# Kernel optimization log

Hardware: AMD Instinct MI355X
Metric: run time of the kernel (lower is better)

## Reference

```python
import jax, jax.numpy as jnp
import numpy as np

B, S, D = 2, 1024, 1024
L, E, F = 2, 8, 2048


def setup_inputs() -> dict:
    key = jax.random.key(0)
    kx, kp, k1, k2 = jax.random.split(key, 4)
    x = jax.random.normal(kx, (B, S, D), dtype=jnp.float32)
    # prototypes scaled so dot products are O(1), keeping softmax well-behaved
    protos = jax.random.normal(kp, (L, E, D), dtype=jnp.float32) / np.sqrt(D)
    W1 = jax.random.normal(k1, (L, E, D, F), dtype=jnp.float32) * 0.02
    W2 = jax.random.normal(k2, (L, E, F, D), dtype=jnp.float32) * 0.02
    return {"x": x, "protos": protos, "W1": W1, "W2": W2, "k": 2}


def _route(x, protos_l, k):
    # expert_mapping: abs(dot(prototype, input)) per expert, keep top-k, rest -> -inf, softmax
    scores = jnp.abs(jnp.einsum("bsd,ed->bse", x, protos_l))  # [B,S,E]
    topv, _ = jax.lax.top_k(scores, k)
    thresh = topv[..., -1:]  # k-th largest per token
    masked = jnp.where(scores >= thresh, scores, -jnp.inf)
    return jax.nn.softmax(masked, axis=-1)  # [B,S,E]


def reference(x, protos, W1, W2, k):
    n_layers = protos.shape[0]
    for l in range(n_layers):  # fixed small layer loop
        w = _route(x, protos[l], k)  # [B,S,E]
        h = jax.nn.relu(jnp.einsum("bsd,edf->bsef", x, W1[l]))  # [B,S,E,F]
        y = jnp.einsum("bsef,efd,bse->bsd", h, W2[l], w)  # weighted expert mix
        x = x + y
    return x
```

## Files before the change

### kernel.cpp

```cpp
#include <hip/hip_runtime.h>
#include <hip/hip_bf16.h>
#include <cstdint>

#define T_TOKENS 2048
#define DDIM 1024
#define FDIM 2048
#define NEXP 8
#define NLAYER 2
#define BMPAD 64
#define RMAX 4608
#define RALLOC 4736

#define ATILE_EL 2048
#define BTILE_EL 4096

typedef unsigned short u16;
typedef short bf16x8 __attribute__((ext_vector_type(8)));
typedef u16 u16x8 __attribute__((ext_vector_type(8)));
typedef u16 u16x4v __attribute__((ext_vector_type(4)));
typedef float f32x4 __attribute__((ext_vector_type(4)));

__device__ __forceinline__ u16 bf16_rn(float f) {
  unsigned u = __builtin_bit_cast(unsigned, f);
  u += 0x7fffu + ((u >> 16) & 1u);
  return (u16)(u >> 16);
}
__device__ __forceinline__ float bf16_f(u16 h) {
  unsigned u = ((unsigned)h) << 16;
  return __builtin_bit_cast(float, u);
}

__device__ __forceinline__ void gl16(const void* g, void* l) {
  __builtin_amdgcn_global_load_lds((const __attribute__((address_space(1))) void*)g,
                                   (__attribute__((address_space(3))) void*)l, 16, 0, 0);
}

__device__ __forceinline__ void xcd_swizzle(int& bx, int& by, int& bz) {
  const unsigned gx = gridDim.x, gy = gridDim.y;
  const unsigned lin = blockIdx.x + gx * (blockIdx.y + gy * blockIdx.z);
  const unsigned nwg = gx * gy * gridDim.z;
  const unsigned nl = (lin & 7u) * (nwg >> 3) + (lin >> 3);
  bx = nl % gx;
  const unsigned t = nl / gx;
  by = t % gy;
  bz = t / gy;
}

__global__ __launch_bounds__(256) void route_kernel(
    const float* __restrict__ x, const float* __restrict__ protos,
    int* __restrict__ eid, float* __restrict__ wgt) {
  const int t = blockIdx.x;
  const int tid = threadIdx.x;
  const float4* xr4 = (const float4*)(x + (size_t)t * DDIM);
  const float4* pr4 = (const float4*)protos;
  __shared__ float red[NEXP][256];
  const float4 xv = xr4[tid];
  float acc[NEXP];
#pragma unroll
  for (int e = 0; e < NEXP; ++e) {
    const float4 p = pr4[e * 256 + tid];
    acc[e] = xv.x * p.x + xv.y * p.y + xv.z * p.z + xv.w * p.w;
  }
#pragma unroll
  for (int e = 0; e < NEXP; ++e) red[e][tid] = acc[e];
  __syncthreads();
  for (int s = 128; s > 0; s >>= 1) {
    if (tid < s) {
#pragma unroll
      for (int e = 0; e < NEXP; ++e) red[e][tid] += red[e][tid + s];
    }
    __syncthreads();
  }
  if (tid == 0) {
    float m1 = -1.f, m2 = -1.f;
    int i1 = 0, i2 = 0;
#pragma unroll
    for (int e = 0; e < NEXP; ++e) {
      float s = fabsf(red[e][0]);
      if (s > m1) { m2 = m1; i2 = i1; m1 = s; i1 = e; }
      else if (s > m2) { m2 = s; i2 = e; }
    }
    float e2 = __expf(m2 - m1);
    float z = 1.f + e2;
    eid[t * 2] = i1;
    eid[t * 2 + 1] = i2;
    wgt[t * 2] = 1.f / z;
    wgt[t * 2 + 1] = e2 / z;
  }
}

__global__ __launch_bounds__(256) void route2_kernel(
    const float* __restrict__ x, const float* __restrict__ protos2,
    const u16* __restrict__ h_hi, const u16* __restrict__ h_lo,
    const float* __restrict__ P, const int* __restrict__ eidA,
    const int* __restrict__ pos, const float* __restrict__ wgtA,
    int* __restrict__ eidB, float* __restrict__ wgtB) {
  const int t = blockIdx.x;
  const int tid = threadIdx.x;
  __shared__ float red[NEXP][256];
  const float4 xv = ((const float4*)(x + (size_t)t * DDIM))[tid];
  float acc[NEXP];
#pragma unroll
  for (int e = 0; e < NEXP; ++e) {
    const float4 p = ((const float4*)protos2)[e * 256 + tid];
    acc[e] = xv.x * p.x + xv.y * p.y + xv.z * p.z + xv.w * p.w;
  }
  const int p0 = pos[t * 2], p1 = pos[t * 2 + 1];
  const int e0 = eidA[t * 2], e1 = eidA[t * 2 + 1];
  const float w0 = wgtA[t * 2], w1 = wgtA[t * 2 + 1];
  const int f0 = tid * 8;
  const int nkbF = FDIM >> 5;
  float h0[8], h1[8];
  {
    const size_t el0 = ((size_t)(p0 >> 6) * nkbF + (f0 >> 5)) * ATILE_EL +
                       (size_t)((((f0 >> 3) & 3) * 64 + (p0 & 63)) * 8);
    const size_t el1 = ((size_t)(p1 >> 6) * nkbF + (f0 >> 5)) * ATILE_EL +
                       (size_t)((((f0 >> 3) & 3) * 64 + (p1 & 63)) * 8);
    u16x8 a = *(const u16x8*)&h_hi[el0], b = *(const u16x8*)&h_lo[el0];
    u16x8 c = *(const u16x8*)&h_hi[el1], d = *(const u16x8*)&h_lo[el1];
#pragma unroll
    for (int j = 0; j < 8; ++j) {
      h0[j] = bf16_f(a[j]) + bf16_f(b[j]);
      h1[j] = bf16_f(c[j]) + bf16_f(d[j]);
    }
  }
#pragma unroll
  for (int e2 = 0; e2 < NEXP; ++e2) {
    const float* P0 = P + ((size_t)(e0 * NEXP + e2)) * FDIM + f0;
    const float* P1 = P + ((size_t)(e1 * NEXP + e2)) * FDIM + f0;
    float c = 0.f;
#pragma unroll
    for (int j = 0; j < 8; ++j) c += w0 * h0[j] * P0[j] + w1 * h1[j] * P1[j];
    acc[e2] += c;
  }
#pragma unroll
  for (int e = 0; e < NEXP; ++e) red[e][tid] = acc[e];
  __syncthreads();
  for (int s = 128; s > 0; s >>= 1) {
    if (tid < s) {
#pragma unroll
      for (int e = 0; e < NEXP; ++e) red[e][tid] += red[e][tid + s];
    }
    __syncthreads();
  }
  if (tid == 0) {
    float m1 = -1.f, m2 = -1.f;
    int i1 = 0, i2 = 0;
#pragma unroll
    for (int e = 0; e < NEXP; ++e) {
      float s = fabsf(red[e][0]);
      if (s > m1) { m2 = m1; i2 = i1; m1 = s; i1 = e; }
      else if (s > m2) { m2 = s; i2 = e; }
    }
    float e2 = __expf(m2 - m1);
    float z = 1.f + e2;
    eidB[t * 2] = i1;
    eidB[t * 2 + 1] = i2;
    wgtB[t * 2] = 1.f / z;
    wgtB[t * 2 + 1] = e2 / z;
  }
}

__global__ __launch_bounds__(256) void compact_kernel(
    const int* __restrict__ eid, int* __restrict__ cnt, int* __restrict__ offp,
    int* __restrict__ row2token, int* __restrict__ pos) {
  __shared__ int lcnt[NEXP][256];
  __shared__ int s_off[NEXP], s_tot[NEXP];
  const int tid = threadIdx.x;
  const int base = tid * 16;

  int my[16];
#pragma unroll
  for (int i = 0; i < 4; ++i)
    *(int4*)&my[i * 4] = *(const int4*)(eid + base + i * 4);

#pragma unroll
  for (int e = 0; e < NEXP; ++e) {
    int c = 0;
#pragma unroll
    for (int i = 0; i < 16; ++i) c += (my[i] == e) ? 1 : 0;
    lcnt[e][tid] = c;
  }

  for (int r = tid; r < RMAX; r += 256) row2token[r] = -1;
  __syncthreads();

  if (tid < NEXP) {
    int run = 0;
    for (int i = 0; i < 256; ++i) {
      int v = lcnt[tid][i];
      lcnt[tid][i] = run;
      run += v;
    }
    s_tot[tid] = run;
  }
  __syncthreads();
  if (tid == 0) {
    int o = 0;
    for (int e = 0; e < NEXP; ++e) {
      s_off[e] = o;
      o += (s_tot[e] + BMPAD - 1) & ~(BMPAD - 1);
    }
  }
  __syncthreads();

  int myoff[NEXP];
#pragma unroll
  for (int e = 0; e < NEXP; ++e) myoff[e] = s_off[e] + lcnt[e][tid];
#pragma unroll
  for (int i = 0; i < 16; ++i) {
    int r = 0;
#pragma unroll
    for (int e = 0; e < NEXP; ++e) r = (my[i] == e) ? myoff[e] : r;
    row2token[r] = (base + i) >> 1;
    pos[base + i] = r;
#pragma unroll
    for (int e = 0; e < NEXP; ++e) myoff[e] += (my[i] == e) ? 1 : 0;
  }

  if (tid < NEXP) {
    cnt[tid] = s_tot[tid];
    offp[tid] = s_off[tid];
  }
}

template <bool LO>
__global__ __launch_bounds__(256) void gather_kernel(
    const float* __restrict__ x, const int* __restrict__ row2token,
    u16* __restrict__ Ahi, u16* __restrict__ Alo) {
  const int r = blockIdx.x;
  const int t = row2token[r];
  const int c = threadIdx.x * 4;
  float4 v = make_float4(0.f, 0.f, 0.f, 0.f);
  if (t >= 0) v = *(const float4*)(x + (size_t)t * DDIM + c);
  float vv[4] = {v.x, v.y, v.z, v.w};
  u16x4v hi, lo;
#pragma unroll
  for (int i = 0; i < 4; ++i) {
    u16 h = bf16_rn(vv[i]);
    hi[i] = h;
    if (LO) lo[i] = bf16_rn(vv[i] - bf16_f(h));
  }
  const size_t el = ((size_t)(r >> 6) * (DDIM >> 5) + (c >> 5)) * ATILE_EL +
                    (size_t)(((c >> 3) & 3) * 64 + (r & 63)) * 8 + (c & 7);
  *(u16x4v*)(Ahi + el) = hi;
  if (LO) *(u16x4v*)(Alo + el) = lo;
}

template <bool LO>
__global__ __launch_bounds__(256) void wconv_kernel(
    const float* __restrict__ W, u16* __restrict__ Hi, u16* __restrict__ Lo,
    int K, int N) {
  const int e = blockIdx.z, nb = blockIdx.x, kb = blockIdx.y;
  const float* Wp = W + ((size_t)e * K + (size_t)kb * 32) * N + nb * 128;
  __shared__ float tile[32][129];
  const int t = threadIdx.x;
#pragma unroll
  for (int i = 0; i < 4; ++i) {
    const int f4 = i * 256 + t;
    const int kr = f4 >> 5;
    const int c4 = (f4 & 31) * 4;
    float4 v = *(const float4*)(Wp + (size_t)kr * N + c4);
    *(float4*)&tile[kr][c4] = v;
  }
  __syncthreads();
  const size_t tb = (((size_t)e * (N >> 7) + nb) * (K >> 5) + kb) * BTILE_EL;
#pragma unroll
  for (int j = 0; j < 2; ++j) {
    const int cid = j * 256 + t;
    const int n = cid & 127, ksel = cid >> 7;
    u16x8 hv, lv;
#pragma unroll
    for (int i = 0; i < 8; ++i) {
      float f = tile[ksel * 8 + i][n];
      u16 h = bf16_rn(f);
      hv[i] = h;
      if (LO) lv[i] = bf16_rn(f - bf16_f(h));
    }
    *(u16x8*)(Hi + tb + (size_t)cid * 8) = hv;
    if (LO) *(u16x8*)(Lo + tb + (size_t)cid * 8) = lv;
  }
}

__global__ __launch_bounds__(256) void wconv_p_kernel(
    const float* __restrict__ W, u16* __restrict__ Hi,
    const float* __restrict__ proto2, float* __restrict__ Ppart, int K, int N) {
  const int e = blockIdx.z, nb = blockIdx.x, kb = blockIdx.y;
  const float* Wp = W + ((size_t)e * K + (size_t)kb * 32) * N + nb * 128;
  __shared__ float tile[32][129];
  __shared__ float pr[NEXP][128];
  const int t = threadIdx.x;
#pragma unroll
  for (int i = 0; i < 4; ++i) {
    const int f4 = i * 256 + t;
    const int kr = f4 >> 5;
    const int c4 = (f4 & 31) * 4;
    float4 v = *(const float4*)(Wp + (size_t)kr * N + c4);
    *(float4*)&tile[kr][c4] = v;
  }
  {
    const int idx = t * 4;
    const int e2 = idx >> 7, n = idx & 127;
    *(float4*)&pr[e2][n] = *(const float4*)(proto2 + (size_t)e2 * DDIM + nb * 128 + n);
  }
  __syncthreads();
  const size_t tb = (((size_t)e * (N >> 7) + nb) * (K >> 5) + kb) * BTILE_EL;
#pragma unroll
  for (int j = 0; j < 2; ++j) {
    const int cid = j * 256 + t;
    const int n = cid & 127, ksel = cid >> 7;
    u16x8 hv;
#pragma unroll
    for (int i = 0; i < 8; ++i) hv[i] = bf16_rn(tile[ksel * 8 + i][n]);
    *(u16x8*)(Hi + tb + (size_t)cid * 8) = hv;
  }
  const int e2 = t >> 5, f = t & 31;
  float s = 0.f;
#pragma unroll 16
  for (int n = 0; n < 128; ++n) s += tile[f][n] * pr[e2][n];
  Ppart[(((size_t)nb * NEXP + e) * NEXP + e2) * FDIM + kb * 32 + f] = s;
}

__global__ __launch_bounds__(256) void reduce_p_kernel(
    const float* __restrict__ Ppart, float* __restrict__ P) {
  const int i = blockIdx.x * 256 + threadIdx.x;
  float s = 0.f;
#pragma unroll
  for (int nb = 0; nb < 8; ++nb) s += Ppart[(size_t)nb * (NEXP * NEXP * FDIM) + i];
  P[i] = s;
}

__global__ __launch_bounds__(256, 3) void gemm_split(
    const u16* __restrict__ Ahi, const u16* __restrict__ Alo,
    const u16* __restrict__ Bhi, const u16* __restrict__ Blo,
    u16* __restrict__ OutHi, u16* __restrict__ OutLo,
    const int* __restrict__ cnt, const int* __restrict__ offp, int K, int N) {
  int bx, by, bz;
  xcd_swizzle(bx, by, bz);
  const int e = bz;
  const int cp = (cnt[e] + 63) & ~63;
  if (by * 64 >= cp) return;
  const int row0 = offp[e] + by * 64;
  const int n0 = bx * 128;
  const int nkb = K >> 5;

  constexpr int BUF_EL = 12288;
  __shared__ u16 lds[2 * BUF_EL];

  const int tid = threadIdx.x;
  const int lane = tid & 63;
  const int wid = tid >> 6;
  const int wr = wid >> 1, wc = wid & 1;
  const int lr = lane & 15, kg = lane >> 4;
  const int lo16 = lane << 4;

  f32x4 acc[2][4];
#pragma unroll
  for (int i = 0; i < 2; ++i)
#pragma unroll
    for (int j = 0; j < 4; ++j)
#pragma unroll
      for (int r = 0; r < 4; ++r) acc[i][j][r] = 0.f;

  const size_t abase = (size_t)(row0 >> 6) * nkb;
  const size_t bbase = ((size_t)e * (N >> 7) + (n0 >> 7)) * nkb;

  auto STAGE = [&](int kb, int b) {
    char* d = (char*)(lds + b * BUF_EL);
    if (wid == 0) {
      const char* gh = (const char*)(Ahi + (abase + kb) * ATILE_EL);
      const char* gl = (const char*)(Alo + (abase + kb) * ATILE_EL);
#pragma unroll
      for (int i = 0; i < 4; ++i) gl16(gh + i * 1024 + lo16, d + i * 1024);
#pragma unroll
      for (int i = 0; i < 4; ++i) gl16(gl + i * 1024 + lo16, d + 4096 + i * 1024);
    } else if (wid == 1) {
      const char* g = (const char*)(Bhi + (bbase + kb) * BTILE_EL);
#pragma unroll
      for (int i = 0; i < 8; ++i) gl16(g + i * 1024 + lo16, d + 8192 + i * 1024);
    } else if (wid == 2) {
      const char* g = (const char*)(Blo + (bbase + kb) * BTILE_EL);
#pragma unroll
      for (int i = 0; i < 8; ++i) gl16(g + i * 1024 + lo16, d + 16384 + i * 1024);
    }
  };

  STAGE(0, 0);
  __syncthreads();

  int cur = 0;
  for (int kb = 0; kb < nkb; ++kb) {
    if (kb + 1 < nkb) STAGE(kb + 1, cur ^ 1);

    const u16* buf = lds + cur * BUF_EL;
    const u16* AsH = buf;
    const u16* AsL = buf + 2048;
    const u16* BsH = buf + 4096;
    const u16* BsL = buf + 8192;
    const int arow = (kg * 64 + wr * 32 + lr) * 8;
    const int bcol = (kg * 128 + wc * 64 + lr) * 8;

    bf16x8 ah0 = *(const bf16x8*)&AsH[arow];
    bf16x8 ah1 = *(const bf16x8*)&AsH[arow + 128];
    bf16x8 bh[4];
#pragma unroll
    for (int j = 0; j < 4; ++j) bh[j] = *(const bf16x8*)&BsH[bcol + j * 128];
#pragma unroll
    for (int j = 0; j < 4; ++j) {
      acc[0][j] = __builtin_amdgcn_mfma_f32_16x16x32_bf16(ah0, bh[j], acc[0][j], 0, 0, 0);
      acc[1][j] = __builtin_amdgcn_mfma_f32_16x16x32_bf16(ah1, bh[j], acc[1][j], 0, 0, 0);
    }
    bf16x8 al0 = *(const bf16x8*)&AsL[arow];
    bf16x8 al1 = *(const bf16x8*)&AsL[arow + 128];
#pragma unroll
    for (int j = 0; j < 4; ++j) {
      bf16x8 bl = *(const bf16x8*)&BsL[bcol + j * 128];
      acc[0][j] = __builtin_amdgcn_mfma_f32_16x16x32_bf16(ah0, bl, acc[0][j], 0, 0, 0);
      acc[1][j] = __builtin_amdgcn_mfma_f32_16x16x32_bf16(ah1, bl, acc[1][j], 0, 0, 0);
      acc[0][j] = __builtin_amdgcn_mfma_f32_16x16x32_bf16(al0, bh[j], acc[0][j], 0, 0, 0);
      acc[1][j] = __builtin_amdgcn_mfma_f32_16x16x32_bf16(al1, bh[j], acc[1][j], 0, 0, 0);
    }
    __syncthreads();
    cur ^= 1;
  }

  const int nkbO = N >> 5;
#pragma unroll
  for (int i = 0; i < 2; ++i) {
#pragma unroll
    for (int j = 0; j < 4; ++j) {
      const int Cj = n0 + wc * 64 + j * 16 + lr;
      f32x4 v = acc[i][j];
#pragma unroll
      for (int r = 0; r < 4; ++r) {
        const int R = row0 + wr * 32 + i * 16 + kg * 4 + r;
        float f = fmaxf(v[r], 0.f);
        const size_t el = ((size_t)(R >> 6) * nkbO + (Cj >> 5)) * ATILE_EL +
                          (size_t)(((Cj >> 3) & 3) * 64 + (R & 63)) * 8 + (Cj & 7);
        u16 h = bf16_rn(f);
        OutHi[el] = h;
        OutLo[el] = bf16_rn(f - bf16_f(h));
      }
    }
  }
}

template <bool RELU, int OUTMODE, int SKF>
__global__ __launch_bounds__(256, 4) void gemm_plain(
    const u16* __restrict__ Ahi, const u16* __restrict__ Bhi,
    u16* __restrict__ OutHi, float* __restrict__ OutF,
    const int* __restrict__ cnt, const int* __restrict__ offp, int K, int N) {
  int bx, by, bz;
  xcd_swizzle(bx, by, bz);
  const int e = bz / SKF, sk = bz % SKF;
  const int cp = (cnt[e] + 63) & ~63;
  if (by * 128 >= cp) return;
  const int row0 = offp[e] + by * 128;
  const int rend = offp[e] + cp;
  const int n0 = bx * 128;
  const int nkb = K >> 5;
  const int kbN = nkb / SKF;
  const int kb0 = sk * kbN;

  constexpr int BUF_EL = 8192;
  __shared__ u16 lds[2 * BUF_EL];

  const int tid = threadIdx.x;
  const int lane = tid & 63;
  const int wid = tid >> 6;
  const int wr = wid >> 1, wc = wid & 1;
  const int lr = lane & 15, kg = lane >> 4;
  const int lo16 = lane << 4;

  f32x4 acc[4][4];
#pragma unroll
  for (int i = 0; i < 4; ++i)
#pragma unroll
    for (int j = 0; j < 4; ++j)
#pragma unroll
      for (int r = 0; r < 4; ++r) acc[i][j][r] = 0.f;

  const int at0 = row0 >> 6;
  const size_t bbase = ((size_t)e * (N >> 7) + (n0 >> 7)) * nkb;

  auto STAGE = [&](int kb, int b) {
    char* d = (char*)(lds + b * BUF_EL);
    if (wid < 2) {
      const char* g = (const char*)(Ahi + ((size_t)(at0 + wid) * nkb + kb) * ATILE_EL);
#pragma unroll
      for (int i = 0; i < 4; ++i) gl16(g + i * 1024 + lo16, d + wid * 4096 + i * 1024);
    } else {
      const char* g = (const char*)(Bhi + (bbase + kb) * BTILE_EL) + (wid - 2) * 4096;
#pragma unroll
      for (int i = 0; i < 4; ++i) gl16(g + i * 1024 + lo16, d + 8192 + (wid - 2) * 4096 + i * 1024);
    }
  };

  STAGE(kb0, 0);
  __syncthreads();

  int cur = 0;
  for (int kb = kb0; kb < kb0 + kbN; ++kb) {
    if (kb + 1 < kb0 + kbN) STAGE(kb + 1, cur ^ 1);

    const u16* buf = lds + cur * BUF_EL;
    const u16* AsH = buf + wr * 2048;
    const u16* BsH = buf + 4096;
    const int arow = (kg * 64 + lr) * 8;
    const int bcol = (kg * 128 + wc * 64 + lr) * 8;

    bf16x8 ah[4], bh[4];
#pragma unroll
    for (int i = 0; i < 4; ++i) ah[i] = *(const bf16x8*)&AsH[arow + i * 128];
#pragma unroll
    for (int j = 0; j < 4; ++j) bh[j] = *(const bf16x8*)&BsH[bcol + j * 128];
#pragma unroll
    for (int i = 0; i < 4; ++i)
#pragma unroll
      for (int j = 0; j < 4; ++j)
        acc[i][j] = __builtin_amdgcn_mfma_f32_16x16x32_bf16(ah[i], bh[j], acc[i][j], 0, 0, 0);
    __syncthreads();
    cur ^= 1;
  }

  const int nkbO = N >> 5;
#pragma unroll
  for (int i = 0; i < 4; ++i) {
#pragma unroll
    for (int j = 0; j < 4; ++j) {
      const int Cj = n0 + wc * 64 + j * 16 + lr;
      f32x4 v = acc[i][j];
#pragma unroll
      for (int r = 0; r < 4; ++r) {
        const int R = row0 + wr * 64 + i * 16 + kg * 4 + r;
        if (R >= rend) continue;
        float f = v[r];
        if (RELU) f = fmaxf(f, 0.f);
        if constexpr (OUTMODE == 0) {
          OutF[((size_t)sk * RALLOC + R) * N + Cj] = f;
        } else {
          const size_t el = ((size_t)(R >> 6) * nkbO + (Cj >> 5)) * ATILE_EL +
                            (size_t)(((Cj >> 3) & 3) * 64 + (R & 63)) * 8 + (Cj & 7);
          OutHi[el] = bf16_rn(f);
        }
      }
    }
  }
}

__global__ __launch_bounds__(256) void apply_kernel(
    const float* __restrict__ part, const int* __restrict__ pos,
    const float* __restrict__ wgt, float* __restrict__ x) {
  const int t = blockIdx.x;
  const int c = threadIdx.x * 4;
  const int p0 = pos[t * 2], p1 = pos[t * 2 + 1];
  const float w0 = wgt[t * 2], w1 = wgt[t * 2 + 1];
  const float* P1p = part + (size_t)RALLOC * DDIM;
  float4 xa = *(float4*)(x + (size_t)t * DDIM + c);
  float4 y0 = *(const float4*)(part + (size_t)p0 * DDIM + c);
  float4 y1 = *(const float4*)(part + (size_t)p1 * DDIM + c);
  const float4 b0 = *(const float4*)(P1p + (size_t)p0 * DDIM + c);
  const float4 b1 = *(const float4*)(P1p + (size_t)p1 * DDIM + c);
  y0.x += b0.x; y0.y += b0.y; y0.z += b0.z; y0.w += b0.w;
  y1.x += b1.x; y1.y += b1.y; y1.z += b1.z; y1.w += b1.w;
  xa.x += w0 * y0.x + w1 * y1.x;
  xa.y += w0 * y0.y + w1 * y1.y;
  xa.z += w0 * y0.z + w1 * y1.z;
  xa.w += w0 * y0.w + w1 * y1.w;
  *(float4*)(x + (size_t)t * DDIM + c) = xa;
}

extern "C" void kernel_launch(void* const* d_in, const int* in_sizes, int n_in,
                              void* d_out, int out_size, void* d_ws, size_t ws_size,
                              hipStream_t stream) {
  const float* x = (const float*)d_in[0];
  const float* protos = (const float*)d_in[1];
  const float* W1 = (const float*)d_in[2];
  const float* W2 = (const float*)d_in[3];
  float* xcur = (float*)d_out;

  u16* W_hi = (u16*)d_ws;
  u16* W_lo = W_hi + (size_t)NEXP * DDIM * FDIM;
  u16* Ag_hi = W_lo + (size_t)NEXP * DDIM * FDIM;
  u16* Ag_lo = Ag_hi + (size_t)RALLOC * DDIM;
  u16* h_hi = Ag_lo + (size_t)RALLOC * DDIM;
  u16* h_lo = h_hi + (size_t)RALLOC * FDIM;
  float* part = (float*)(h_lo + (size_t)RALLOC * FDIM);
  float* Ppart = part + (size_t)2 * RALLOC * DDIM;
  float* P = Ppart + (size_t)8 * NEXP * NEXP * FDIM;
  float* wgtA = P + (size_t)NEXP * NEXP * FDIM;
  float* wgtB = wgtA + T_TOKENS * 2;
  int* eidA = (int*)(wgtB + T_TOKENS * 2);
  int* eidB = eidA + T_TOKENS * 2;
  int* posA = eidB + T_TOKENS * 2;
  int* posB = posA + T_TOKENS * 2;
  int* cnt = posB + T_TOKENS * 2;
  int* offp = cnt + NEXP;
  int* row2token = offp + NEXP;

  hipMemcpyAsync(xcur, x, (size_t)T_TOKENS * DDIM * sizeof(float),
                 hipMemcpyDeviceToDevice, stream);

  const float* protos2 = protos + (size_t)NEXP * DDIM;

  route_kernel<<<T_TOKENS, 256, 0, stream>>>(xcur, protos, eidA, wgtA);
  compact_kernel<<<1, 256, 0, stream>>>(eidA, cnt, offp, row2token, posA);
  gather_kernel<true><<<RMAX, 256, 0, stream>>>(xcur, row2token, Ag_hi, Ag_lo);
  wconv_kernel<true><<<dim3(FDIM / 128, DDIM / 32, NEXP), 256, 0, stream>>>(
      W1, W_hi, W_lo, DDIM, FDIM);
  gemm_split<<<dim3(FDIM / 128, RMAX / 64, NEXP), 256, 0, stream>>>(
      Ag_hi, Ag_lo, W_hi, W_lo, h_hi, h_lo, cnt, offp, DDIM, FDIM);
  wconv_p_kernel<<<dim3(DDIM / 128, FDIM / 32, NEXP), 256, 0, stream>>>(
      W2, W_hi, protos2, Ppart, FDIM, DDIM);
  reduce_p_kernel<<<NEXP * NEXP * FDIM / 256, 256, 0, stream>>>(Ppart, P);
  gemm_plain<false, 0, 2><<<dim3(DDIM / 128, RMAX / 128, NEXP * 2), 256, 0, stream>>>(
      h_hi, W_hi, nullptr, part, cnt, offp, FDIM, DDIM);
  route2_kernel<<<T_TOKENS, 256, 0, stream>>>(
      xcur, protos2, h_hi, h_lo, P, eidA, posA, wgtA, eidB, wgtB);
  apply_kernel<<<T_TOKENS, 256, 0, stream>>>(part, posA, wgtA, xcur);

  compact_kernel<<<1, 256, 0, stream>>>(eidB, cnt, offp, row2token, posB);
  gather_kernel<false><<<RMAX, 256, 0, stream>>>(xcur, row2token, Ag_hi, nullptr);
  wconv_kernel<false><<<dim3(FDIM / 128, DDIM / 32, NEXP), 256, 0, stream>>>(
      W1 + (size_t)NEXP * DDIM * FDIM, W_hi, nullptr, DDIM, FDIM);
  gemm_plain<true, 2, 1><<<dim3(FDIM / 128, RMAX / 128, NEXP), 256, 0, stream>>>(
      Ag_hi, W_hi, h_hi, nullptr, cnt, offp, DDIM, FDIM);
  wconv_kernel<false><<<dim3(DDIM / 128, FDIM / 32, NEXP), 256, 0, stream>>>(
      W2 + (size_t)NEXP * FDIM * DDIM, W_hi, nullptr, FDIM, DDIM);
  gemm_plain<false, 0, 2><<<dim3(DDIM / 128, RMAX / 128, NEXP * 2), 256, 0, stream>>>(
      h_hi, W_hi, nullptr, part, cnt, offp, FDIM, DDIM);
  apply_kernel<<<T_TOKENS, 256, 0, stream>>>(part, posB, wgtB, xcur);
}
```

Before: 366.7 us.

## Balance async LDS staging across all waves and use partial vmcnt waits

The tile-loading work in both GEMM kernels is spread evenly across all four waves, each issuing the same number of global-to-LDS loads, where before one wave carried the A load and three carried uneven B loads. __syncthreads is replaced with explicit s_waitcnt vmcnt(N) plus raw s_barrier and sched barriers. This lets the next stage's prefetch stay in flight while the current buffer is consumed, instead of draining all outstanding loads at each barrier. It depends on the vmcnt counts being exactly right; a wrong count would race on LDS.

```diff
diff --git a/kernel.cpp b/kernel.cpp
--- a/kernel.cpp
+++ b/kernel.cpp
@@ -19,6 +19,10 @@
 typedef u16 u16x8 __attribute__((ext_vector_type(8)));
 typedef u16 u16x4v __attribute__((ext_vector_type(4)));
 typedef float f32x4 __attribute__((ext_vector_type(4)));
+
+#define VMCNT(n) asm volatile("s_waitcnt vmcnt(" #n ")" ::: "memory")
+#define SB() __builtin_amdgcn_sched_barrier(0)
+#define BAR() __builtin_amdgcn_s_barrier()
 
 __device__ __forceinline__ u16 bf16_rn(float f) {
   unsigned u = __builtin_bit_cast(unsigned, f);
@@ -367,30 +371,48 @@
 
   auto STAGE = [&](int kb, int b) {
     char* d = (char*)(lds + b * BUF_EL);
+    const char* gah = (const char*)(Ahi + (abase + kb) * ATILE_EL);
+    const char* gal = (const char*)(Alo + (abase + kb) * ATILE_EL);
+    const char* gbh = (const char*)(Bhi + (bbase + kb) * BTILE_EL);
+    const char* gbl = (const char*)(Blo + (bbase + kb) * BTILE_EL);
     if (wid == 0) {
-      const char* gh = (const char*)(Ahi + (abase + kb) * ATILE_EL);
-      const char* gl = (const char*)(Alo + (abase + kb) * ATILE_EL);
-#pragma unroll
-      for (int i = 0; i < 4; ++i) gl16(gh + i * 1024 + lo16, d + i * 1024);
-#pragma unroll
-      for (int i = 0; i < 4; ++i) gl16(gl + i * 1024 + lo16, d + 4096 + i * 1024);
+      gl16(gah + 0 * 1024 + lo16, d + 0 * 1024);
+      gl16(gah + 1 * 1024 + lo16, d + 1 * 1024);
+      gl16(gah + 2 * 1024 + lo16, d + 2 * 1024);
+      gl16(gah + 3 * 1024 + lo16, d + 3 * 1024);
+      gl16(gal + 0 * 1024 + lo16, d + 4096 + 0 * 1024);
+      gl16(gal + 1 * 1024 + lo16, d + 4096 + 1 * 1024);
     } else if (wid == 1) {
-      const char* g = (const char*)(Bhi + (bbase + kb) * BTILE_EL);
-#pragma unroll
-      for (int i = 0; i < 8; ++i) gl16(g + i * 1024 + lo16, d + 8192 + i * 1024);
+      gl16(gal + 2 * 1024 + lo16, d + 4096 + 2 * 1024);
+      gl16(gal + 3 * 1024 + lo16, d + 4096 + 3 * 1024);
+      gl16(gbh + 0 * 1024 + lo16, d + 8192 + 0 * 1024);
+      gl16(gbh + 1 * 1024 + lo16, d + 8192 + 1 * 1024);
+      gl16(gbh + 2 * 1024 + lo16, d + 8192 + 2 * 1024);
+      gl16(gbh + 3 * 1024 + lo16, d + 8192 + 3 * 1024);
     } else if (wid == 2) {
-      const char* g = (const char*)(Blo + (bbase + kb) * BTILE_EL);
-#pragma unroll
-      for (int i = 0; i < 8; ++i) gl16(g + i * 1024 + lo16, d + 16384 + i * 1024);
+      gl16(gbh + 4 * 1024 + lo16, d + 8192 + 4 * 1024);
+      gl16(gbh + 5 * 1024 + lo16, d + 8192 + 5 * 1024);
+      gl16(gbh + 6 * 1024 + lo16, d + 8192 + 6 * 1024);
+      gl16(gbh + 7 * 1024 + lo16, d + 8192 + 7 * 1024);
+      gl16(gbl + 0 * 1024 + lo16, d + 16384 + 0 * 1024);
+      gl16(gbl + 1 * 1024 + lo16, d + 16384 + 1 * 1024);
+    } else {
+      gl16(gbl + 2 * 1024 + lo16, d + 16384 + 2 * 1024);
+      gl16(gbl + 3 * 1024 + lo16, d + 16384 + 3 * 1024);
+      gl16(gbl + 4 * 1024 + lo16, d + 16384 + 4 * 1024);
+      gl16(gbl + 5 * 1024 + lo16, d + 16384 + 5 * 1024);
+      gl16(gbl + 6 * 1024 + lo16, d + 16384 + 6 * 1024);
+      gl16(gbl + 7 * 1024 + lo16, d + 16384 + 7 * 1024);
     }
   };
 
   STAGE(0, 0);
-  __syncthreads();
-
   int cur = 0;
   for (int kb = 0; kb < nkb; ++kb) {
-    if (kb + 1 < nkb) STAGE(kb + 1, cur ^ 1);
+    const bool pf = (kb + 1 < nkb);
+    if (pf) STAGE(kb + 1, cur ^ 1);
+    if (pf) { VMCNT(6); } else { VMCNT(0); }
+    SB(); BAR(); SB();
 
     const u16* buf = lds + cur * BUF_EL;
     const u16* AsH = buf;
@@ -420,7 +442,7 @@
       acc[0][j] = __builtin_amdgcn_mfma_f32_16x16x32_bf16(al0, bh[j], acc[0][j], 0, 0, 0);
       acc[1][j] = __builtin_amdgcn_mfma_f32_16x16x32_bf16(al1, bh[j], acc[1][j], 0, 0, 0);
     }
-    __syncthreads();
+    SB(); BAR(); SB();
     cur ^= 1;
   }
 
@@ -487,21 +509,26 @@
     char* d = (char*)(lds + b * BUF_EL);
     if (wid < 2) {
       const char* g = (const char*)(Ahi + ((size_t)(at0 + wid) * nkb + kb) * ATILE_EL);
-#pragma unroll
-      for (int i = 0; i < 4; ++i) gl16(g + i * 1024 + lo16, d + wid * 4096 + i * 1024);
+      gl16(g + 0 * 1024 + lo16, d + wid * 4096 + 0 * 1024);
+      gl16(g + 1 * 1024 + lo16, d + wid * 4096 + 1 * 1024);
+      gl16(g + 2 * 1024 + lo16, d + wid * 4096 + 2 * 1024);
+      gl16(g + 3 * 1024 + lo16, d + wid * 4096 + 3 * 1024);
     } else {
       const char* g = (const char*)(Bhi + (bbase + kb) * BTILE_EL) + (wid - 2) * 4096;
-#pragma unroll
-      for (int i = 0; i < 4; ++i) gl16(g + i * 1024 + lo16, d + 8192 + (wid - 2) * 4096 + i * 1024);
+      gl16(g + 0 * 1024 + lo16, d + 8192 + (wid - 2) * 4096 + 0 * 1024);
+      gl16(g + 1 * 1024 + lo16, d + 8192 + (wid - 2) * 4096 + 1 * 1024);
+      gl16(g + 2 * 1024 + lo16, d + 8192 + (wid - 2) * 4096 + 2 * 1024);
+      gl16(g + 3 * 1024 + lo16, d + 8192 + (wid - 2) * 4096 + 3 * 1024);
     }
   };
 
   STAGE(kb0, 0);
-  __syncthreads();
-
   int cur = 0;
   for (int kb = kb0; kb < kb0 + kbN; ++kb) {
-    if (kb + 1 < kb0 + kbN) STAGE(kb + 1, cur ^ 1);
+    const bool pf = (kb + 1 < kb0 + kbN);
+    if (pf) STAGE(kb + 1, cur ^ 1);
+    if (pf) { VMCNT(4); } else { VMCNT(0); }
+    SB(); BAR(); SB();
 
     const u16* buf = lds + cur * BUF_EL;
     const u16* AsH = buf + wr * 2048;
@@ -519,7 +546,7 @@
 #pragma unroll
       for (int j = 0; j < 4; ++j)
         acc[i][j] = __builtin_amdgcn_mfma_f32_16x16x32_bf16(ah[i], bh[j], acc[i][j], 0, 0, 0);
-    __syncthreads();
+    SB(); BAR(); SB();
     cur ^= 1;
   }
 
```

Result: faster. 357.2 us (-2.6%).
